# Kernel optimization log

Measured on AMD Instinct MI355X. Metric: run time of the kernel, lower is better.

Reference implementation:

```python
import jax, jax.numpy as jnp
import numpy as np

EPS_RMS = 1e-4   # RunningMeanStd epsilon (mean=0, var=1 at init)
LN_EPS = 1e-5    # torch LayerNorm default
NUM_HEADS = 16


def _layernorm(x, g, b):
    m = x.mean(-1, keepdims=True)
    v = ((x - m) ** 2).mean(-1, keepdims=True)
    return (x - m) / jnp.sqrt(v + LN_EPS) * g + b


def _rms_normalize(a):
    # RunningMeanStd.normalize with mean=0, var=1: clip(a / sqrt(1+eps), -5, 5)
    return jnp.clip(a / jnp.sqrt(1.0 + EPS_RMS), -5.0, 5.0)


def _sinusoidal_pe(pos, d):
    # pos [...,] -> [..., d]; matches torch code: div_term over arange(d//2)
    div = jnp.exp(jnp.arange(d // 2, dtype=jnp.float32) * (-np.log(1000.0) / d))
    ang = pos[..., None] * div                         # [..., d//2]
    pe = jnp.zeros(pos.shape + (d,), dtype=jnp.float32)
    pe = pe.at[..., 0::2].set(jnp.sin(ang))
    pe = pe.at[..., 1::2].set(jnp.cos(ang))
    return pe


def _encoder_layer(xs, mask, Wqkv, bqkv, Wo, bo, g1, be1, g2, be2, Wf1, bf1, Wf2, bf2):
    # post-LN TransformerEncoderLayer with boolean attention mask [B,S,S]
    B, S, D = xs.shape
    hd = D // NUM_HEADS
    qkv = xs @ Wqkv.T + bqkv                           # [B,S,3D]
    q, k, v = jnp.split(qkv, 3, axis=-1)
    q = q.reshape(B, S, NUM_HEADS, hd).transpose(0, 2, 1, 3)
    k = k.reshape(B, S, NUM_HEADS, hd).transpose(0, 2, 1, 3)
    v = v.reshape(B, S, NUM_HEADS, hd).transpose(0, 2, 1, 3)
    scores = jnp.einsum('bhqd,bhkd->bhqk', q, k) / jnp.sqrt(jnp.float32(hd))
    scores = jnp.where(mask[:, None, :, :], -jnp.inf, scores)
    attn = jax.nn.softmax(scores, axis=-1)
    o = jnp.einsum('bhqk,bhkd->bhqd', attn, v).transpose(0, 2, 1, 3).reshape(B, S, D)
    o = o @ Wo.T + bo
    xs = _layernorm(xs + o, g1, be1)
    ff = jax.nn.gelu(xs @ Wf1.T + bf1, approximate=False) @ Wf2.T + bf2
    xs = _layernorm(xs + ff, g2, be2)
    return xs


def reference(x, w, y, W_nail, b_nail, W_cond, b_cond, Wqkv, bqkv, Wo, bo,
              ln1_g, ln1_b, ln2_g, ln2_b, W1, b1, W2, b2, W_ham, b_ham):
    B, Lx = x.shape[0], x.shape[1]
    n_w = w.shape[1] * w.shape[2]
    L = Lx + n_w + 1                                   # total_paragraph_length
    S = L - 1
    D = W_nail.shape[0]

    w_last = w[:, -1]                                  # [B, P, 6]

    # embed_x
    t = jnp.nan_to_num(x[..., 0])
    xc = jnp.nan_to_num(x)
    xx = _rms_normalize(xc)[..., 1:] @ W_nail.T + b_nail   # [B,Lx,D]
    xx = xx + _sinusoidal_pe(t, D)
    x_mask = jnp.isnan(x[..., 0])                      # [B,Lx]

    # embed_w
    wc = jnp.nan_to_num(w)
    wn = _rms_normalize(wc).reshape(B, -1, w.shape[-1])    # [B,Lw*P,6]
    ww = wn @ W_cond.T + b_cond                        # [B,Lw*P,D]

    tgt = jnp.concatenate([xx, ww], axis=1)            # [B,S,D]

    # custom per-batch boolean mask: causal, but columns [0,Lx) follow x padding mask
    causal = jnp.triu(jnp.ones((S, S), dtype=bool), 1)
    mask = jnp.broadcast_to(causal, (B, S, S))
    mask = mask.at[:, :, :Lx].set(x_mask[:, None, :])

    # global positional encoding added only on the w-token segment
    pe_g = _sinusoidal_pe(jnp.arange(L, dtype=jnp.float32), D)  # [L,D]
    tgt = tgt.at[:, Lx:].add(pe_g[Lx:L - 1])

    for i in range(Wqkv.shape[0]):
        tgt = _encoder_layer(tgt, mask, Wqkv[i], bqkv[i], Wo[i], bo[i],
                             ln1_g[i], ln1_b[i], ln2_g[i], ln2_b[i],
                             W1[i], b1[i], W2[i], b2[i])

    y_resid_hat = (tgt[:, -1] @ W_ham.T + b_ham).reshape(B, -1, 6)
    y_resid = jax.lax.stop_gradient(y - w_last)
    loss = jnp.mean((y_resid_hat - y_resid) ** 2)
    return loss


def setup_inputs() -> dict:
    key = jax.random.key(0)
    ks = jax.random.split(key, 16)
    NL, D, FF, HAM = 4, 1024, 4096, 144
    s = 0.02
    return {
        'x': jax.random.normal(ks[0], (8, 512, 64), jnp.float32),
        'w': jax.random.normal(ks[1], (8, 16, 24, 6), jnp.float32),
        'y': jax.random.normal(ks[2], (8, 24, 6), jnp.float32),
        'W_nail': jax.random.normal(ks[3], (D, 63), jnp.float32) * s,
        'b_nail': jnp.zeros((D,), jnp.float32),
        'W_cond': jax.random.normal(ks[4], (D, 6), jnp.float32) * s,
        'b_cond': jnp.zeros((D,), jnp.float32),
        'Wqkv': jax.random.normal(ks[5], (NL, 3 * D, D), jnp.float32) * s,
        'bqkv': jnp.zeros((NL, 3 * D), jnp.float32),
        'Wo': jax.random.normal(ks[6], (NL, D, D), jnp.float32) * s,
        'bo': jnp.zeros((NL, D), jnp.float32),
        'ln1_g': jnp.ones((NL, D), jnp.float32),
        'ln1_b': jnp.zeros((NL, D), jnp.float32),
        'ln2_g': jnp.ones((NL, D), jnp.float32),
        'ln2_b': jnp.zeros((NL, D), jnp.float32),
        'W1': jax.random.normal(ks[7], (NL, FF, D), jnp.float32) * s,
        'b1': jnp.zeros((NL, FF), jnp.float32),
        'W2': jax.random.normal(ks[8], (NL, D, FF), jnp.float32) * s,
        'b2': jnp.zeros((NL, D), jnp.float32),
        'W_ham': jax.random.normal(ks[9], (HAM, D), jnp.float32) * s,
        'b_ham': jnp.zeros((HAM,), jnp.float32),
    }
```

## Files before the change

kernel.cpp:

```cpp
#include <hip/hip_runtime.h>
#include <math.h>


#define B_      8
#define LX_     512
#define NW_     384
#define S_      896
#define D_      1024
#define H_      16
#define HD_     64
#define FF_     4096
#define HAM_    144

#define RMS_SCALE 0.9999500037496876f
#define PE_C     (-6.907755278982137f / 1024.0f)

typedef __bf16 bf16x4 __attribute__((ext_vector_type(4)));
typedef __bf16 bf16x8 __attribute__((ext_vector_type(8)));
typedef float  f32x4  __attribute__((ext_vector_type(4)));

static __device__ __forceinline__ float nan0(float v) { return (v != v) ? 0.0f : v; }

static __device__ __forceinline__ void async_copy16(const __bf16* g, __bf16* l) {
    __builtin_amdgcn_global_load_lds(
        (const __attribute__((address_space(1))) void*)g,
        (__attribute__((address_space(3))) void*)l, 16, 0, 0);
}

static __device__ __forceinline__ float fast_gelu(float x) {
    float x3 = x * x * x;
    float z = 0.7978845608028654f * x + 0.035677408136300125f * x3;
    float az = fabsf(z);
    float e = __expf(2.0f * az);
    float t = 1.0f - 2.0f / (e + 1.0f);
    t = (z < 0.0f) ? -t : t;
    return 0.5f * x * (1.0f + t);
}

__global__ __launch_bounds__(256) void convert4_kernel(
        const float* __restrict__ s0, const float* __restrict__ s1,
        const float* __restrict__ s2, const float* __restrict__ s3,
        __bf16* __restrict__ d0, __bf16* __restrict__ d1,
        __bf16* __restrict__ d2, __bf16* __restrict__ d3) {
    int blk = blockIdx.x;
    const float* src; __bf16* dst; int base;
    if (blk < 3072)      { src = s0; dst = d0; base = blk; }
    else if (blk < 4096) { src = s1; dst = d1; base = blk - 3072; }
    else if (blk < 8192) { src = s2; dst = d2; base = blk - 4096; }
    else                 { src = s3; dst = d3; base = blk - 8192; }
    int i = (base * 256 + threadIdx.x) * 4;
    float4 v = *(const float4*)&src[i];
    bf16x4 o = {(__bf16)v.x, (__bf16)v.y, (__bf16)v.z, (__bf16)v.w};
    *(bf16x4*)&dst[i] = o;
}

__global__ __launch_bounds__(256) void transpose_nail_kernel(
        const float* __restrict__ W_nail, float* __restrict__ WT) {
    int i = blockIdx.x * 256 + threadIdx.x;
    int d = i & 1023, kk = i >> 10;
    WT[kk * 1024 + d] = W_nail[d * 63 + kk];
}

__global__ __launch_bounds__(256) void embed_x_kernel(
        const float* __restrict__ x, const float* __restrict__ WT,
        const float* __restrict__ b_nail, __bf16* __restrict__ tgt_bf,
        int* __restrict__ xmask) {
    int row0 = blockIdx.x * 8;
    int tid = threadIdx.x;
    __shared__ float xn[8][64];
    __shared__ float ts[8];
#pragma unroll
    for (int it = 0; it < 2; ++it) {
        int i = tid + it * 256;
        int r = i >> 6, c = i & 63;
        float vv = x[(size_t)(row0 + r) * 64 + c];
        float v0 = nan0(vv);
        xn[r][c] = fminf(fmaxf(v0 * RMS_SCALE, -5.0f), 5.0f);
        if (c == 0) { ts[r] = v0; xmask[row0 + r] = (vv != vv) ? 1 : 0; }
    }
    __syncthreads();
    int d0 = tid * 4;
    float4 bz = *(const float4*)&b_nail[d0];
    float acc[8][4];
#pragma unroll
    for (int r = 0; r < 8; ++r) {
        acc[r][0] = bz.x; acc[r][1] = bz.y; acc[r][2] = bz.z; acc[r][3] = bz.w;
    }
    for (int k = 0; k < 63; ++k) {
        float4 wv = *(const float4*)&WT[k * 1024 + d0];
#pragma unroll
        for (int r = 0; r < 8; ++r) {
            float xv = xn[r][k + 1];
            acc[r][0] += xv * wv.x; acc[r][1] += xv * wv.y;
            acc[r][2] += xv * wv.z; acc[r][3] += xv * wv.w;
        }
    }
    float div[4];
#pragma unroll
    for (int j = 0; j < 4; ++j)
        div[j] = __expf((float)((d0 + j) >> 1) * PE_C);
#pragma unroll
    for (int r = 0; r < 8; ++r) {
        int row = row0 + r;
        int b = row >> 9, i = row & 511;
        float t = ts[r];
        bf16x4 ob;
#pragma unroll
        for (int j = 0; j < 4; ++j) {
            float ang = t * div[j];
            float pe = ((d0 + j) & 1) ? __cosf(ang) : __sinf(ang);
            ob[j] = (__bf16)(acc[r][j] + pe);
        }
        *(bf16x4*)&tgt_bf[((size_t)b * S_ + i) * D_ + d0] = ob;
    }
}

__global__ __launch_bounds__(256) void embed_w_kernel(
        const float* __restrict__ w, const float* __restrict__ W_cond,
        const float* __restrict__ b_cond, __bf16* __restrict__ tgt_bf) {
    int row = blockIdx.x;
    int b = row / NW_, j = row % NW_;
    const float* wr = w + (long)row * 6;
    float wn[6];
#pragma unroll
    for (int k = 0; k < 6; ++k)
        wn[k] = fminf(fmaxf(nan0(wr[k]) * RMS_SCALE, -5.0f), 5.0f);
    int tid = threadIdx.x;
    int d0 = tid * 4;
    float pos = (float)(LX_ + j);
    bf16x4 ob;
#pragma unroll
    for (int jj = 0; jj < 4; ++jj) {
        int d = d0 + jj;
        float acc = b_cond[d];
        const float* wc = W_cond + (long)d * 6;
#pragma unroll
        for (int k = 0; k < 6; ++k) acc += wn[k] * wc[k];
        float dv = expf((float)(d >> 1) * PE_C);
        float ang = pos * dv;
        ob[jj] = (__bf16)(acc + ((d & 1) ? cosf(ang) : sinf(ang)));
    }
    *(bf16x4*)&tgt_bf[((long)b * S_ + LX_ + j) * D_ + d0] = ob;
}


#define LDA(BUF, MH) do {                                                      \
    _Pragma("unroll")                                                          \
    for (int i_ = 0; i_ < 4; ++i_) {                                           \
        const int row_ = (MH) * 128 + wr * 64 + i_ * 16 + frow;                \
        _Pragma("unroll")                                                      \
        for (int k_ = 0; k_ < 2; ++k_)                                         \
            a[i_][k_] = *(const bf16x8*)&As[BUF][row_ * 64 +                   \
                (((quad + k_ * 4) ^ sf) * 8)];                                 \
    }                                                                          \
} while (0)

#define LDB(BUF, NH) do {                                                      \
    _Pragma("unroll")                                                          \
    for (int j_ = 0; j_ < NJ; ++j_) {                                          \
        const int row_ = (BN == 256)                                           \
            ? ((NH) * 128 + j_ * 16 + wc * 32 + frow)                          \
            : ((NH) * 64 + wc * 16 + frow);                                    \
        _Pragma("unroll")                                                      \
        for (int k_ = 0; k_ < 2; ++k_)                                         \
            b[(NH) * NJ + j_][k_] = *(const bf16x8*)&Bs[BUF][row_ * 64 +       \
                (((quad + k_ * 4) ^ sf) * 8)];                                 \
    }                                                                          \
} while (0)

#define MMA(MH, NH) do {                                                       \
    _Pragma("unroll")                                                          \
    for (int i_ = 0; i_ < 4; ++i_)                                             \
        _Pragma("unroll")                                                      \
        for (int j_ = 0; j_ < NJ; ++j_)                                        \
            _Pragma("unroll")                                                  \
            for (int k_ = 0; k_ < 2; ++k_)                                     \
                acc[(MH) * 4 + i_][(NH) * NJ + j_] =                           \
                    __builtin_amdgcn_mfma_f32_16x16x32_bf16(                   \
                        b[(NH) * NJ + j_][k_], a[i_][k_],                      \
                        acc[(MH) * 4 + i_][(NH) * NJ + j_], 0, 0, 0);          \
} while (0)

#define STAGE_A(BUF, H, KT) do {                                               \
    const __bf16* g_ = Ag + (size_t)((H) * 128) * K + ((size_t)(KT) << 6);     \
    async_copy16(g_, &As[BUF][((H) * 128) * 64 + dst8]);                       \
    async_copy16(g_ + ((size_t)K << 6), &As[BUF][((H) * 128 + 64) * 64 + dst8]); \
} while (0)

#define STAGE_B(BUF, H, KT) do {                                               \
    if constexpr (BN == 256) {                                                 \
        const __bf16* g_ = Wg + (size_t)((H) * 128) * K + ((size_t)(KT) << 6); \
        async_copy16(g_, &Bs[BUF][((H) * 128) * 64 + dst8]);                   \
        async_copy16(g_ + ((size_t)K << 6),                                    \
                     &Bs[BUF][((H) * 128 + 64) * 64 + dst8]);                  \
    } else {                                                                   \
        const __bf16* g_ = Wg + (size_t)((H) * 64) * K + ((size_t)(KT) << 6);  \
        async_copy16(g_, &Bs[BUF][((H) * 64) * 64 + dst8]);                    \
    }                                                                          \
} while (0)

#define PHASE_SYNC() do {                                                      \
    __builtin_amdgcn_sched_barrier(0);                                         \
    __builtin_amdgcn_s_barrier();                                              \
    asm volatile("s_waitcnt lgkmcnt(0)" ::: "memory");                         \
    __builtin_amdgcn_sched_barrier(0);                                         \
} while (0)

#define PHASE_END() do {                                                       \
    __builtin_amdgcn_sched_barrier(0);                                         \
    __builtin_amdgcn_s_barrier();                                              \
} while (0)

#define VM_MAIN do {                                                           \
    if constexpr (BN == 256) { asm volatile("s_waitcnt vmcnt(6)" ::: "memory"); } \
    else                     { asm volatile("s_waitcnt vmcnt(4)" ::: "memory"); } \
} while (0)
#define VM_ZERO asm volatile("s_waitcnt vmcnt(0)" ::: "memory")
#define VM_NONE ((void)0)

#define GTILE(S1, S2, VMOP) do {                                               \
    const int bf_ = t & 1;                                                     \
    LDA(bf_, 0); LDB(bf_, 0);                                                  \
    if (S1) STAGE_A(bf_ ^ 1, 1, t + 1);                                        \
    PHASE_SYNC();                                                              \
    __builtin_amdgcn_s_setprio(1); MMA(0, 0); __builtin_amdgcn_s_setprio(0);   \
    PHASE_END();                                                               \
    LDB(bf_, 1);                                                               \
    if (S2) STAGE_B(bf_, 0, t + 2);                                            \
    PHASE_SYNC();                                                              \
    __builtin_amdgcn_s_setprio(1); MMA(0, 1); __builtin_amdgcn_s_setprio(0);   \
    PHASE_END();                                                               \
    LDA(bf_, 1);                                                               \
    if (S2) STAGE_A(bf_, 0, t + 2);                                            \
    PHASE_SYNC();                                                              \
    __builtin_amdgcn_s_setprio(1); MMA(1, 0); __builtin_amdgcn_s_setprio(0);   \
    PHASE_END();                                                               \
    if (S2) STAGE_B(bf_, 1, t + 2);                                            \
    VMOP;                                                                      \
    PHASE_SYNC();                                                              \
    __builtin_amdgcn_s_setprio(1); MMA(1, 1); __builtin_amdgcn_s_setprio(0);   \
    PHASE_END();                                                               \
} while (0)

template <int BN, int MODE>
__global__ __launch_bounds__(512, 2) void gemm8p(
        const __bf16* __restrict__ A, const __bf16* __restrict__ W,
        const float* __restrict__ bias,
        __bf16* __restrict__ Cb,
        __bf16* __restrict__ Cq, __bf16* __restrict__ Ck, __bf16* __restrict__ Cv,
        int M, int N, int K) {
    constexpr int NI = BN / 64;
    constexpr int NJ = NI / 2;
    static_assert(BN == 256 || BN == 128, "BN");
    __shared__ __attribute__((aligned(16))) __bf16 As[2][256 * 64];
    __shared__ __attribute__((aligned(16))) __bf16 Bs[2][BN * 64];

    const int tid = threadIdx.x;
    const int wave = tid >> 6, lane = tid & 63;
    const int wr = wave >> 2, wc = wave & 3;
    const int frow = lane & 15, quad = lane >> 4;
    const int sf = frow & 7;
    const int m0 = blockIdx.y * 256, n0 = blockIdx.x * BN;

    const int sr = tid >> 3;
    const int scol = ((tid & 7) ^ (sr & 7)) * 8;
    const __bf16* Ag = A + (size_t)(m0 + sr) * K + scol;
    const __bf16* Wg = W + (size_t)(n0 + sr) * K + scol;
    const int dst8 = tid * 8;

    f32x4 acc[8][NI];
#pragma unroll
    for (int i = 0; i < 8; ++i)
#pragma unroll
        for (int j = 0; j < NI; ++j) acc[i][j] = 0.0f;
    bf16x8 a[4][2];
    bf16x8 b[NI][2];

    const int NT = K >> 6;

    STAGE_B(0, 0, 0); STAGE_A(0, 0, 0); STAGE_B(0, 1, 0); STAGE_A(0, 1, 0);
    STAGE_B(1, 0, 1); STAGE_A(1, 0, 1); STAGE_B(1, 1, 1);
    VM_MAIN;
    __builtin_amdgcn_s_barrier();

    int t = 0;
    for (; t < NT - 2; ++t) { GTILE(1, 1, VM_MAIN); }
    GTILE(1, 0, VM_ZERO);
    ++t;
    GTILE(0, 0, VM_NONE);

#pragma unroll
    for (int ni = 0; ni < NI; ++ni) {
        int cg0;
        if constexpr (BN == 256)
            cg0 = n0 + (ni >> 1) * 128 + (ni & 1) * 16 + wc * 32 + quad * 4;
        else
            cg0 = n0 + ni * 64 + wc * 16 + quad * 4;
        float4 bv = *(const float4*)&bias[cg0];
        float bz[4] = {bv.x, bv.y, bv.z, bv.w};
#pragma unroll
        for (int mi = 0; mi < 8; ++mi) {
            int rg = m0 + (mi >> 2) * 128 + wr * 64 + (mi & 3) * 16 + frow;
            float vv[4];
#pragma unroll
            for (int r = 0; r < 4; ++r) {
                float v = acc[mi][ni][r] + bz[r];
                if (MODE == 1) v = fast_gelu(v);
                vv[r] = v;
            }
            if (MODE == 2) {
                int which = cg0 >> 10;
                int h = (cg0 & 1023) >> 6;
                int e = cg0 & 63;
                int bb = rg / S_, s = rg % S_;
                if (which == 2) {
                    size_t vb = ((size_t)bb * H_ + h) * HD_ + e;
#pragma unroll
                    for (int r = 0; r < 4; ++r)
                        Cv[(vb + r) * S_ + s] = (__bf16)vv[r];
                } else {
                    bf16x4 o = {(__bf16)vv[0], (__bf16)vv[1], (__bf16)vv[2], (__bf16)vv[3]};
                    __bf16* dstp = (which == 0) ? Cq : Ck;
                    *(bf16x4*)&dstp[(((size_t)bb * H_ + h) * S_ + s) * HD_ + e] = o;
                }
            } else {
                bf16x4 o = {(__bf16)vv[0], (__bf16)vv[1], (__bf16)vv[2], (__bf16)vv[3]};
                *(bf16x4*)&Cb[(size_t)rg * N + cg0] = o;
            }
        }
    }
}

__global__ __launch_bounds__(512, 2) void gemm2p(
        const __bf16* __restrict__ A, const __bf16* __restrict__ W,
        const float* __restrict__ bias, __bf16* __restrict__ Cb,
        int M, int N, int K) {
    constexpr int BN = 128;
    constexpr int NI = 2, NJ = 1;
    __shared__ __attribute__((aligned(16))) __bf16 As[2][256 * 64];
    __shared__ __attribute__((aligned(16))) __bf16 Bs[2][128 * 64];

    const int tid = threadIdx.x;
    const int wave = tid >> 6, lane = tid & 63;
    const int wr = wave >> 2, wc = wave & 3;
    const int frow = lane & 15, quad = lane >> 4;
    const int sf = frow & 7;

    const int nwg = gridDim.x * gridDim.y;
    int orig = blockIdx.y * gridDim.x + blockIdx.x;
    int tile = orig;
    if ((nwg & 7) == 0) tile = (orig & 7) * (nwg >> 3) + (orig >> 3);
    const int m0 = (tile / gridDim.x) * 256;
    const int n0 = (tile % gridDim.x) * BN;

    const int sr = tid >> 3;
    const int scol = ((tid & 7) ^ (sr & 7)) * 8;
    const __bf16* Ag = A + (size_t)(m0 + sr) * K + scol;
    const __bf16* Wg = W + (size_t)(n0 + sr) * K + scol;
    const int dst8 = tid * 8;

    f32x4 acc[8][NI];
#pragma unroll
    for (int i = 0; i < 8; ++i)
#pragma unroll
        for (int j = 0; j < NI; ++j) acc[i][j] = 0.0f;
    bf16x8 a[4][2];
    bf16x8 b[NI][2];

    const int NT = K >> 6;

#define VM4 asm volatile("s_waitcnt vmcnt(4)" ::: "memory")
#define GTILE2(S1, S2, VMOP) do {                                              \
    const int bf_ = t & 1;                                                     \
            \
    LDA(bf_, 0); LDB(bf_, 0); LDB(bf_, 1);                                     \
    if (S1) STAGE_A(bf_ ^ 1, 1, t + 1);                                        \
    PHASE_SYNC();                                                              \
    __builtin_amdgcn_s_setprio(1); MMA(0, 0); MMA(0, 1);                       \
    __builtin_amdgcn_s_setprio(0);                                             \
    PHASE_END();                                                               \
      \
    LDA(bf_, 1);                                                               \
    if (S2) { STAGE_B(bf_, 0, t + 2); STAGE_B(bf_, 1, t + 2);                  \
              STAGE_A(bf_, 0, t + 2); }                                        \
    VMOP;                                                                      \
    PHASE_SYNC();                                                              \
    __builtin_amdgcn_s_setprio(1); MMA(1, 0); MMA(1, 1);                       \
    __builtin_amdgcn_s_setprio(0);                                             \
    PHASE_END();                                                               \
} while (0)

    STAGE_B(0, 0, 0); STAGE_B(0, 1, 0); STAGE_A(0, 0, 0); STAGE_A(0, 1, 0);
    STAGE_B(1, 0, 1); STAGE_B(1, 1, 1); STAGE_A(1, 0, 1);
    VM4;
    __builtin_amdgcn_s_barrier();

    int t = 0;
    for (; t < NT - 2; ++t) { GTILE2(1, 1, VM4); }
    GTILE2(1, 0, VM_ZERO);
    ++t;
    GTILE2(0, 0, VM_NONE);
#undef GTILE2
#undef VM4

#pragma unroll
    for (int ni = 0; ni < NI; ++ni) {
        int cg0 = n0 + ni * 64 + wc * 16 + quad * 4;
        float4 bv = *(const float4*)&bias[cg0];
        float bz[4] = {bv.x, bv.y, bv.z, bv.w};
#pragma unroll
        for (int mi = 0; mi < 8; ++mi) {
            int rg = m0 + (mi >> 2) * 128 + wr * 64 + (mi & 3) * 16 + frow;
            bf16x4 o;
#pragma unroll
            for (int r = 0; r < 4; ++r) o[r] = (__bf16)(acc[mi][ni][r] + bz[r]);
            *(bf16x4*)&Cb[(size_t)rg * N + cg0] = o;
        }
    }
}

__global__ __launch_bounds__(256) void attn_mfma(
        const __bf16* __restrict__ q, const __bf16* __restrict__ k,
        const __bf16* __restrict__ vt, const int* __restrict__ xmask,
        __bf16* __restrict__ ctx) {
    __shared__ __attribute__((aligned(16))) __bf16 Ks[2][64 * 64];
    __shared__ __attribute__((aligned(16))) __bf16 Vs[2][64 * 64];
    __shared__ __attribute__((aligned(16))) __bf16 Ps[4][16 * 64];
    __shared__ float mb[LX_];
    int tid = threadIdx.x;
    int wave = tid >> 6, lane = tid & 63;
    int frow = lane & 15, quad = lane >> 4;
    int f7 = frow & 7, f3 = frow >> 3;
    int sl0 = (quad ^ f7) * 8;
    int sl1 = ((quad + 4) ^ f7) * 8;

    int blk = blockIdx.x;
    int xcd = blk & 7, slot = blk >> 3;
    int bh = xcd * 16 + slot / 14;
    int qt = slot % 14;
    int b = bh >> 4, h = bh & 15;
    int q0 = qt * 64;
    int q0w = q0 + wave * 16;
    size_t base = (size_t)bh * S_ * HD_;
    size_t vbase = (size_t)bh * HD_ * S_;

    for (int i = tid; i < LX_; i += 256)
        mb[i] = xmask[(b << 9) + i] ? -INFINITY : 0.0f;

    const __bf16* qrow = q + base + (size_t)(q0w + frow) * HD_ + quad * 8;
    bf16x8 aq0 = *(const bf16x8*)qrow;
    bf16x8 aq1 = *(const bf16x8*)(qrow + 32);

    f32x4 o[4];
#pragma unroll
    for (int dt = 0; dt < 4; ++dt) o[dt] = 0.0f;
    float mrow[4] = {-INFINITY, -INFINITY, -INFINITY, -INFINITY};
    float lrow[4] = {0.0f, 0.0f, 0.0f, 0.0f};

    int kend = (q0 >= LX_) ? (q0 + 64) : LX_;
    int NT = kend >> 6;

    int srow = tid >> 3;
    int kcol = ((tid & 7) ^ (srow & 7)) * 8;
    const __bf16* kg = k + base + (size_t)srow * HD_ + kcol;
    const __bf16* vg = vt + vbase + (size_t)srow * S_ + kcol;

#define ASTAGE(BUF, K0) do {                                                   \
    const __bf16* kg_ = kg + (size_t)(K0) * HD_;                               \
    async_copy16(kg_,                  &Ks[BUF][tid * 8]);                     \
    async_copy16(kg_ + 32 * HD_,       &Ks[BUF][2048 + tid * 8]);              \
    const __bf16* vg_ = vg + (K0);                                             \
    async_copy16(vg_,                  &Vs[BUF][tid * 8]);                     \
    async_copy16(vg_ + 32 * S_,        &Vs[BUF][2048 + tid * 8]);              \
} while (0)

    ASTAGE(0, 0);
    __syncthreads();

    for (int t = 0; t < NT; ++t) {
        int buf = t & 1;
        int k0 = t << 6;
        if (t + 1 < NT) {
            ASTAGE(buf ^ 1, k0 + 64);
            asm volatile("s_waitcnt vmcnt(4)" ::: "memory");
        } else {
            asm volatile("s_waitcnt vmcnt(0)" ::: "memory");
        }
        __builtin_amdgcn_s_barrier();
        __builtin_amdgcn_sched_barrier(0);

        f32x4 scr[4];
        __builtin_amdgcn_s_setprio(1);
#pragma unroll
        for (int nt = 0; nt < 4; ++nt) {
            int row = (nt * 16 + frow) * 64;
            bf16x8 bk0 = *(const bf16x8*)&Ks[buf][row + sl0];
            bf16x8 bk1 = *(const bf16x8*)&Ks[buf][row + sl1];
            f32x4 z = 0.0f;
            z = __builtin_amdgcn_mfma_f32_16x16x32_bf16(aq0, bk0, z, 0, 0, 0);
            z = __builtin_amdgcn_mfma_f32_16x16x32_bf16(aq1, bk1, z, 0, 0, 0);
            scr[nt] = z;
        }
        __builtin_amdgcn_s_setprio(0);

        float tmax[4] = {-INFINITY, -INFINITY, -INFINITY, -INFINITY};
#pragma unroll
        for (int nt = 0; nt < 4; ++nt) {
            int kj = k0 + nt * 16 + frow;
            float bias = (kj < LX_) ? mb[kj] : 0.0f;
#pragma unroll
            for (int r = 0; r < 4; ++r) {
                float s = scr[nt][r] * 0.125f + bias;
                if (kj >= LX_ && kj > q0w + quad * 4 + r) s = -INFINITY;
                scr[nt][r] = s;
                tmax[r] = fmaxf(tmax[r], s);
            }
        }
#pragma unroll
        for (int off = 1; off < 16; off <<= 1)
#pragma unroll
            for (int r = 0; r < 4; ++r)
                tmax[r] = fmaxf(tmax[r], __shfl_xor(tmax[r], off, 64));

        float alpha[4], rsum[4];
#pragma unroll
        for (int r = 0; r < 4; ++r) {
            float nm = fmaxf(mrow[r], tmax[r]);
            alpha[r] = (nm == -INFINITY) ? 1.0f : __expf(mrow[r] - nm);
            mrow[r] = nm;
            rsum[r] = 0.0f;
        }
#pragma unroll
        for (int nt = 0; nt < 4; ++nt) {
#pragma unroll
            for (int r = 0; r < 4; ++r) {
                float s = scr[nt][r];
                float p = (s == -INFINITY) ? 0.0f : __expf(s - mrow[r]);
                rsum[r] += p;
                int ql = quad * 4 + r;
                int pslot = ((nt * 2 + f3) ^ (ql & 7)) * 8 + f7;
                Ps[wave][ql * 64 + pslot] = (__bf16)p;
            }
        }
#pragma unroll
        for (int off = 1; off < 16; off <<= 1)
#pragma unroll
            for (int r = 0; r < 4; ++r)
                rsum[r] += __shfl_xor(rsum[r], off, 64);
#pragma unroll
        for (int r = 0; r < 4; ++r)
            lrow[r] = lrow[r] * alpha[r] + rsum[r];
#pragma unroll
        for (int dt = 0; dt < 4; ++dt)
#pragma unroll
            for (int r = 0; r < 4; ++r)
                o[dt][r] *= alpha[r];

        bf16x8 ap0 = *(const bf16x8*)&Ps[wave][frow * 64 + sl0];
        bf16x8 ap1 = *(const bf16x8*)&Ps[wave][frow * 64 + sl1];
        __builtin_amdgcn_s_setprio(1);
#pragma unroll
        for (int dt = 0; dt < 4; ++dt) {
            int row = (dt * 16 + frow) * 64;
            bf16x8 bv0 = *(const bf16x8*)&Vs[buf][row + sl0];
            bf16x8 bv1 = *(const bf16x8*)&Vs[buf][row + sl1];
            o[dt] = __builtin_amdgcn_mfma_f32_16x16x32_bf16(ap0, bv0, o[dt], 0, 0, 0);
            o[dt] = __builtin_amdgcn_mfma_f32_16x16x32_bf16(ap1, bv1, o[dt], 0, 0, 0);
        }
        __builtin_amdgcn_s_setprio(0);
        __builtin_amdgcn_sched_barrier(0);
        __builtin_amdgcn_s_barrier();
    }
#undef ASTAGE

#pragma unroll
    for (int r = 0; r < 4; ++r) {
        float inv = (lrow[r] > 0.0f) ? 1.0f / lrow[r] : 0.0f;
        int qg = q0w + quad * 4 + r;
        size_t ob = ((size_t)b * S_ + qg) * D_ + h * HD_;
#pragma unroll
        for (int dt = 0; dt < 4; ++dt)
            ctx[ob + dt * 16 + frow] = (__bf16)(o[dt][r] * inv);
    }
}

__global__ __launch_bounds__(256) void add_ln_kernel(
        __bf16* __restrict__ xs_bf, const __bf16* __restrict__ o,
        const float* __restrict__ g, const float* __restrict__ bb) {
    long row = blockIdx.x;
    __bf16* xr = xs_bf + row * D_;
    const __bf16* orr = o + row * D_;
    int tid = threadIdx.x;
    bf16x4 a4 = *(const bf16x4*)&xr[tid * 4];
    bf16x4 b4v = *(const bf16x4*)&orr[tid * 4];
    float vv[4];
#pragma unroll
    for (int j = 0; j < 4; ++j) vv[j] = (float)a4[j] + (float)b4v[j];
    float s = vv[0] + vv[1] + vv[2] + vv[3];
    __shared__ float red[4];
    __shared__ float stat;
#pragma unroll
    for (int off = 32; off; off >>= 1) s += __shfl_down(s, off, 64);
    if ((tid & 63) == 0) red[tid >> 6] = s;
    __syncthreads();
    if (tid == 0) stat = (red[0] + red[1] + red[2] + red[3]) * (1.0f / 1024.0f);
    __syncthreads();
    float mean = stat;
    float d[4];
    float s2 = 0.0f;
#pragma unroll
    for (int j = 0; j < 4; ++j) { d[j] = vv[j] - mean; s2 += d[j] * d[j]; }
    __syncthreads();
#pragma unroll
    for (int off = 32; off; off >>= 1) s2 += __shfl_down(s2, off, 64);
    if ((tid & 63) == 0) red[tid >> 6] = s2;
    __syncthreads();
    if (tid == 0) stat = (red[0] + red[1] + red[2] + red[3]) * (1.0f / 1024.0f);
    __syncthreads();
    float inv = 1.0f / sqrtf(stat + 1e-5f);
    float4 gg = *(const float4*)&g[tid * 4];
    float4 bv = *(const float4*)&bb[tid * 4];
    float g4[4] = {gg.x, gg.y, gg.z, gg.w};
    float b4[4] = {bv.x, bv.y, bv.z, bv.w};
    bf16x4 ob;
#pragma unroll
    for (int j = 0; j < 4; ++j) ob[j] = (__bf16)(d[j] * inv * g4[j] + b4[j]);
    *(bf16x4*)&xr[tid * 4] = ob;
}

__global__ __launch_bounds__(256) void head_kernel(
        const __bf16* __restrict__ tgt_bf, const float* __restrict__ W_ham,
        const float* __restrict__ b_ham, float* __restrict__ out) {
    int b = blockIdx.x;
    int tid = threadIdx.x;
    __shared__ float xr[D_];
    const __bf16* row = tgt_bf + ((long)b * S_ + (S_ - 1)) * D_;
    for (int i = tid; i < D_; i += 256) xr[i] = (float)row[i];
    __syncthreads();
    for (int n = tid; n < HAM_; n += 256) {
        float acc = b_ham[n];
        const float* wr = W_ham + (long)n * D_;
        for (int kk = 0; kk < D_; ++kk) acc += xr[kk] * wr[kk];
        out[b * HAM_ + n] = acc;
    }
}

__global__ __launch_bounds__(256) void loss_kernel(
        const float* __restrict__ head_out, const float* __restrict__ y,
        const float* __restrict__ w, float* __restrict__ out) {
    int tid = threadIdx.x;
    float acc = 0.0f;
    for (int i = tid; i < B_ * HAM_; i += 256) {
        int b = i / HAM_, r = i % HAM_;
        float w_last = w[((long)b * 16 + 15) * HAM_ + r];
        float resid = y[i] - w_last;
        float dd = head_out[i] - resid;
        acc += dd * dd;
    }
    __shared__ float red[4];
#pragma unroll
    for (int off = 32; off; off >>= 1) acc += __shfl_down(acc, off, 64);
    if ((tid & 63) == 0) red[tid >> 6] = acc;
    __syncthreads();
    if (tid == 0)
        out[0] = (red[0] + red[1] + red[2] + red[3]) * (1.0f / (B_ * HAM_));
}

extern "C" void kernel_launch(void* const* d_in, const int* in_sizes, int n_in,
                              void* d_out, int out_size, void* d_ws, size_t ws_size,
                              hipStream_t stream) {
    const float* x      = (const float*)d_in[0];
    const float* w      = (const float*)d_in[1];
    const float* y      = (const float*)d_in[2];
    const float* W_nail = (const float*)d_in[3];
    const float* b_nail = (const float*)d_in[4];
    const float* W_cond = (const float*)d_in[5];
    const float* b_cond = (const float*)d_in[6];
    const float* Wqkv   = (const float*)d_in[7];
    const float* bqkv   = (const float*)d_in[8];
    const float* Wo     = (const float*)d_in[9];
    const float* bo     = (const float*)d_in[10];
    const float* ln1_g  = (const float*)d_in[11];
    const float* ln1_b  = (const float*)d_in[12];
    const float* ln2_g  = (const float*)d_in[13];
    const float* ln2_b  = (const float*)d_in[14];
    const float* W1     = (const float*)d_in[15];
    const float* b1     = (const float*)d_in[16];
    const float* W2     = (const float*)d_in[17];
    const float* b2     = (const float*)d_in[18];
    const float* W_ham  = (const float*)d_in[19];
    const float* b_ham  = (const float*)d_in[20];

    float* ws = (float*)d_ws;
    const long SEG = (long)B_ * S_ * D_;
    float*  W_nailT = ws;
    __bf16* tmp_bf = (__bf16*)(ws + SEG);
    __bf16* tgt_bf = (__bf16*)(ws + 2 * SEG);
    __bf16* ctx_bf = (__bf16*)(ws + 2 * SEG + SEG / 2);
    __bf16* qb     = (__bf16*)(ws + 3 * SEG);
    __bf16* kb     = (__bf16*)(ws + 3 * SEG + SEG / 2);
    __bf16* vb     = (__bf16*)(ws + 4 * SEG);
    __bf16* ffh_bf = (__bf16*)(ws + 2 * SEG + SEG / 2);
    __bf16* wbf    = (__bf16*)(ws + 4 * SEG + SEG / 2);
    int*    xmask    = (int*)(ws + 4 * SEG + SEG / 2 + 6291456);
    float*  head_out = ws + 4 * SEG + SEG / 2 + 6291456 + 4096;

    __bf16* wqkv_bf = wbf;
    __bf16* wo_bf   = wbf + 3145728;
    __bf16* w1_bf   = wbf + 4194304;
    __bf16* w2_bf   = wbf + 8388608;

    const int M = B_ * S_;

    transpose_nail_kernel<<<252, 256, 0, stream>>>(W_nail, W_nailT);
    embed_x_kernel<<<B_ * LX_ / 8, 256, 0, stream>>>(x, W_nailT, b_nail, tgt_bf, xmask);
    embed_w_kernel<<<B_ * NW_, 256, 0, stream>>>(w, W_cond, b_cond, tgt_bf);

    for (int L = 0; L < 4; ++L) {
        const int NQ = 3 * D_ * D_, NO = D_ * D_, N1 = FF_ * D_, N2 = D_ * FF_;
        convert4_kernel<<<12288, 256, 0, stream>>>(
            Wqkv + (size_t)L * NQ, Wo + (size_t)L * NO,
            W1 + (size_t)L * N1, W2 + (size_t)L * N2,
            wqkv_bf, wo_bf, w1_bf, w2_bf);

        gemm8p<256, 2><<<dim3(3 * D_ / 256, M / 256), 512, 0, stream>>>(
            tgt_bf, wqkv_bf, bqkv + (size_t)L * 3 * D_,
            nullptr, qb, kb, vb, M, 3 * D_, D_);
        attn_mfma<<<B_ * H_ * (S_ / 64), 256, 0, stream>>>(qb, kb, vb, xmask, ctx_bf);
        gemm2p<<<dim3(D_ / 128, M / 256), 512, 0, stream>>>(
            ctx_bf, wo_bf, bo + (size_t)L * D_, tmp_bf, M, D_, D_);
        add_ln_kernel<<<M, 256, 0, stream>>>(tgt_bf, tmp_bf,
            ln1_g + (size_t)L * D_, ln1_b + (size_t)L * D_);
        gemm8p<256, 1><<<dim3(FF_ / 256, M / 256), 512, 0, stream>>>(
            tgt_bf, w1_bf, b1 + (size_t)L * FF_,
            ffh_bf, nullptr, nullptr, nullptr, M, FF_, D_);
        gemm2p<<<dim3(D_ / 128, M / 256), 512, 0, stream>>>(
            ffh_bf, w2_bf, b2 + (size_t)L * D_, tmp_bf, M, D_, FF_);
        add_ln_kernel<<<M, 256, 0, stream>>>(tgt_bf, tmp_bf,
            ln2_g + (size_t)L * D_, ln2_b + (size_t)L * D_);
    }

    head_kernel<<<B_, 256, 0, stream>>>(tgt_bf, W_ham, b_ham, head_out);
    loss_kernel<<<1, 256, 0, stream>>>(head_out, y, w, (float*)d_out);
}
```

Before: 1.663 ms.

## Load attention K/V straight from global into registers, drop LDS staging

The attention kernel no longer stages K and V tiles through double-buffered shared memory with async copies and block barriers. Each wave now loads its K and V fragments directly from global memory into registers every tile. The mask/causal handling is split into three specialised paths (masked prefix, unmasked, diagonal), and launch bounds now request 3 blocks per CU. This removes LDS traffic and per-tile barriers, but each of the four waves re-reads the same K/V from global/L2 with no prefetch overlap.

```diff
diff --git a/kernel.cpp b/kernel.cpp
--- a/kernel.cpp
+++ b/kernel.cpp
@@ -372,14 +372,12 @@
 #define VM4 asm volatile("s_waitcnt vmcnt(4)" ::: "memory")
 #define GTILE2(S1, S2, VMOP) do {                                              \
     const int bf_ = t & 1;                                                     \
-            \
     LDA(bf_, 0); LDB(bf_, 0); LDB(bf_, 1);                                     \
     if (S1) STAGE_A(bf_ ^ 1, 1, t + 1);                                        \
     PHASE_SYNC();                                                              \
     __builtin_amdgcn_s_setprio(1); MMA(0, 0); MMA(0, 1);                       \
     __builtin_amdgcn_s_setprio(0);                                             \
     PHASE_END();                                                               \
-      \
     LDA(bf_, 1);                                                               \
     if (S2) { STAGE_B(bf_, 0, t + 2); STAGE_B(bf_, 1, t + 2);                  \
               STAGE_A(bf_, 0, t + 2); }                                        \
@@ -419,12 +417,10 @@
     }
 }
 
-__global__ __launch_bounds__(256) void attn_mfma(
+__global__ __launch_bounds__(256, 3) void attn_mfma(
         const __bf16* __restrict__ q, const __bf16* __restrict__ k,
         const __bf16* __restrict__ vt, const int* __restrict__ xmask,
         __bf16* __restrict__ ctx) {
-    __shared__ __attribute__((aligned(16))) __bf16 Ks[2][64 * 64];
-    __shared__ __attribute__((aligned(16))) __bf16 Vs[2][64 * 64];
     __shared__ __attribute__((aligned(16))) __bf16 Ps[4][16 * 64];
     __shared__ float mb[LX_];
     int tid = threadIdx.x;
@@ -446,6 +442,7 @@
 
     for (int i = tid; i < LX_; i += 256)
         mb[i] = xmask[(b << 9) + i] ? -INFINITY : 0.0f;
+    __syncthreads();
 
     const __bf16* qrow = q + base + (size_t)(q0w + frow) * HD_ + quad * 8;
     bf16x8 aq0 = *(const bf16x8*)qrow;
@@ -460,60 +457,63 @@
     int kend = (q0 >= LX_) ? (q0 + 64) : LX_;
     int NT = kend >> 6;
 
-    int srow = tid >> 3;
-    int kcol = ((tid & 7) ^ (srow & 7)) * 8;
-    const __bf16* kg = k + base + (size_t)srow * HD_ + kcol;
-    const __bf16* vg = vt + vbase + (size_t)srow * S_ + kcol;
-
-#define ASTAGE(BUF, K0) do {                                                   \
-    const __bf16* kg_ = kg + (size_t)(K0) * HD_;                               \
-    async_copy16(kg_,                  &Ks[BUF][tid * 8]);                     \
-    async_copy16(kg_ + 32 * HD_,       &Ks[BUF][2048 + tid * 8]);              \
-    const __bf16* vg_ = vg + (K0);                                             \
-    async_copy16(vg_,                  &Vs[BUF][tid * 8]);                     \
-    async_copy16(vg_ + 32 * S_,        &Vs[BUF][2048 + tid * 8]);              \
-} while (0)
-
-    ASTAGE(0, 0);
-    __syncthreads();
+    const __bf16* kg = k + base;
+    const __bf16* vg = vt + vbase;
 
     for (int t = 0; t < NT; ++t) {
-        int buf = t & 1;
         int k0 = t << 6;
-        if (t + 1 < NT) {
-            ASTAGE(buf ^ 1, k0 + 64);
-            asm volatile("s_waitcnt vmcnt(4)" ::: "memory");
-        } else {
-            asm volatile("s_waitcnt vmcnt(0)" ::: "memory");
-        }
-        __builtin_amdgcn_s_barrier();
-        __builtin_amdgcn_sched_barrier(0);
+
+        bf16x8 bk[4][2];
+#pragma unroll
+        for (int nt = 0; nt < 4; ++nt) {
+            const __bf16* kr = kg + (size_t)(k0 + nt * 16 + frow) * HD_ + quad * 8;
+            bk[nt][0] = *(const bf16x8*)kr;
+            bk[nt][1] = *(const bf16x8*)(kr + 32);
+        }
 
         f32x4 scr[4];
         __builtin_amdgcn_s_setprio(1);
 #pragma unroll
         for (int nt = 0; nt < 4; ++nt) {
-            int row = (nt * 16 + frow) * 64;
-            bf16x8 bk0 = *(const bf16x8*)&Ks[buf][row + sl0];
-            bf16x8 bk1 = *(const bf16x8*)&Ks[buf][row + sl1];
             f32x4 z = 0.0f;
-            z = __builtin_amdgcn_mfma_f32_16x16x32_bf16(aq0, bk0, z, 0, 0, 0);
-            z = __builtin_amdgcn_mfma_f32_16x16x32_bf16(aq1, bk1, z, 0, 0, 0);
+            z = __builtin_amdgcn_mfma_f32_16x16x32_bf16(aq0, bk[nt][0], z, 0, 0, 0);
+            z = __builtin_amdgcn_mfma_f32_16x16x32_bf16(aq1, bk[nt][1], z, 0, 0, 0);
             scr[nt] = z;
         }
         __builtin_amdgcn_s_setprio(0);
 
         float tmax[4] = {-INFINITY, -INFINITY, -INFINITY, -INFINITY};
-#pragma unroll
-        for (int nt = 0; nt < 4; ++nt) {
-            int kj = k0 + nt * 16 + frow;
-            float bias = (kj < LX_) ? mb[kj] : 0.0f;
-#pragma unroll
-            for (int r = 0; r < 4; ++r) {
-                float s = scr[nt][r] * 0.125f + bias;
-                if (kj >= LX_ && kj > q0w + quad * 4 + r) s = -INFINITY;
-                scr[nt][r] = s;
-                tmax[r] = fmaxf(tmax[r], s);
+        if (k0 + 64 <= LX_) {
+#pragma unroll
+            for (int nt = 0; nt < 4; ++nt) {
+                float bias = mb[k0 + nt * 16 + frow];
+#pragma unroll
+                for (int r = 0; r < 4; ++r) {
+                    float s = scr[nt][r] * 0.125f + bias;
+                    scr[nt][r] = s;
+                    tmax[r] = fmaxf(tmax[r], s);
+                }
+            }
+        } else if (k0 != q0) {
+#pragma unroll
+            for (int nt = 0; nt < 4; ++nt)
+#pragma unroll
+                for (int r = 0; r < 4; ++r) {
+                    float s = scr[nt][r] * 0.125f;
+                    scr[nt][r] = s;
+                    tmax[r] = fmaxf(tmax[r], s);
+                }
+        } else {
+#pragma unroll
+            for (int nt = 0; nt < 4; ++nt) {
+                int kj = k0 + nt * 16 + frow;
+#pragma unroll
+                for (int r = 0; r < 4; ++r) {
+                    float s = scr[nt][r] * 0.125f;
+                    if (kj > q0w + quad * 4 + r) s = -INFINITY;
+                    scr[nt][r] = s;
+                    tmax[r] = fmaxf(tmax[r], s);
+                }
             }
         }
 #pragma unroll
@@ -542,6 +542,15 @@
                 Ps[wave][ql * 64 + pslot] = (__bf16)p;
             }
         }
+
+        bf16x8 bv[4][2];
+#pragma unroll
+        for (int dt = 0; dt < 4; ++dt) {
+            const __bf16* vr = vg + (size_t)(dt * 16 + frow) * S_ + k0 + quad * 8;
+            bv[dt][0] = *(const bf16x8*)vr;
+            bv[dt][1] = *(const bf16x8*)(vr + 32);
+        }
+
 #pragma unroll
         for (int off = 1; off < 16; off <<= 1)
 #pragma unroll
@@ -561,17 +570,11 @@
         __builtin_amdgcn_s_setprio(1);
 #pragma unroll
         for (int dt = 0; dt < 4; ++dt) {
-            int row = (dt * 16 + frow) * 64;
-            bf16x8 bv0 = *(const bf16x8*)&Vs[buf][row + sl0];
-            bf16x8 bv1 = *(const bf16x8*)&Vs[buf][row + sl1];
-            o[dt] = __builtin_amdgcn_mfma_f32_16x16x32_bf16(ap0, bv0, o[dt], 0, 0, 0);
-            o[dt] = __builtin_amdgcn_mfma_f32_16x16x32_bf16(ap1, bv1, o[dt], 0, 0, 0);
+            o[dt] = __builtin_amdgcn_mfma_f32_16x16x32_bf16(ap0, bv[dt][0], o[dt], 0, 0, 0);
+            o[dt] = __builtin_amdgcn_mfma_f32_16x16x32_bf16(ap1, bv[dt][1], o[dt], 0, 0, 0);
         }
         __builtin_amdgcn_s_setprio(0);
-        __builtin_amdgcn_sched_barrier(0);
-        __builtin_amdgcn_s_barrier();
-    }
-#undef ASTAGE
+    }
 
 #pragma unroll
     for (int r = 0; r < 4; ++r) {
```

Result: slower. 1.921 ms (+15.5%).

## Preload both A halves per GEMM k-tile and specialize attention masking paths

Applied to the files above, without the earlier changes.

The GEMM main loop now reads both A halves from LDS into separate register sets at the start of each k-tile. All four next-stage copies are issued after the first MMA phase, which drops one barrier phase per tile and changes the vmcnt wait depth. Separately, the attention score masking is split into three paths (fully-unmasked prefix, off-diagonal, diagonal) to avoid per-element bias and causal checks. This raises register pressure for the extra A fragments and relies on tile alignment assumptions about LX_ and q0 for the causal branches.

```diff
diff --git a/kernel.cpp b/kernel.cpp
--- a/kernel.cpp
+++ b/kernel.cpp
@@ -155,6 +155,17 @@
     }                                                                          \
 } while (0)
 
+#define LDA2(BUF, MH) do {                                                     \
+    _Pragma("unroll")                                                          \
+    for (int i_ = 0; i_ < 4; ++i_) {                                           \
+        const int row_ = (MH) * 128 + wr * 64 + i_ * 16 + frow;                \
+        _Pragma("unroll")                                                      \
+        for (int k_ = 0; k_ < 2; ++k_)                                         \
+            a2[i_][k_] = *(const bf16x8*)&As[BUF][row_ * 64 +                  \
+                (((quad + k_ * 4) ^ sf) * 8)];                                 \
+    }                                                                          \
+} while (0)
+
 #define LDB(BUF, NH) do {                                                      \
     _Pragma("unroll")                                                          \
     for (int j_ = 0; j_ < NJ; ++j_) {                                          \
@@ -178,6 +189,19 @@
                 acc[(MH) * 4 + i_][(NH) * NJ + j_] =                           \
                     __builtin_amdgcn_mfma_f32_16x16x32_bf16(                   \
                         b[(NH) * NJ + j_][k_], a[i_][k_],                      \
+                        acc[(MH) * 4 + i_][(NH) * NJ + j_], 0, 0, 0);          \
+} while (0)
+
+#define MMA2(MH, NH) do {                                                      \
+    _Pragma("unroll")                                                          \
+    for (int i_ = 0; i_ < 4; ++i_)                                             \
+        _Pragma("unroll")                                                      \
+        for (int j_ = 0; j_ < NJ; ++j_)                                        \
+            _Pragma("unroll")                                                  \
+            for (int k_ = 0; k_ < 2; ++k_)                                     \
+                acc[(MH) * 4 + i_][(NH) * NJ + j_] =                           \
+                    __builtin_amdgcn_mfma_f32_16x16x32_bf16(                   \
+                        b[(NH) * NJ + j_][k_], a2[i_][k_],                     \
                         acc[(MH) * 4 + i_][(NH) * NJ + j_], 0, 0, 0);          \
 } while (0)
 
@@ -365,43 +389,41 @@
 #pragma unroll
         for (int j = 0; j < NI; ++j) acc[i][j] = 0.0f;
     bf16x8 a[4][2];
+    bf16x8 a2[4][2];
     bf16x8 b[NI][2];
 
     const int NT = K >> 6;
 
-#define VM4 asm volatile("s_waitcnt vmcnt(4)" ::: "memory")
-#define GTILE2(S1, S2, VMOP) do {                                              \
+#define VM6 asm volatile("s_waitcnt vmcnt(6)" ::: "memory")
+#define GTILE2(S2, VMOP) do {                                                  \
     const int bf_ = t & 1;                                                     \
-            \
-    LDA(bf_, 0); LDB(bf_, 0); LDB(bf_, 1);                                     \
-    if (S1) STAGE_A(bf_ ^ 1, 1, t + 1);                                        \
+                           \
+    LDA(bf_, 0); LDA2(bf_, 1); LDB(bf_, 0); LDB(bf_, 1);                       \
     PHASE_SYNC();                                                              \
     __builtin_amdgcn_s_setprio(1); MMA(0, 0); MMA(0, 1);                       \
     __builtin_amdgcn_s_setprio(0);                                             \
     PHASE_END();                                                               \
-      \
-    LDA(bf_, 1);                                                               \
+       \
     if (S2) { STAGE_B(bf_, 0, t + 2); STAGE_B(bf_, 1, t + 2);                  \
-              STAGE_A(bf_, 0, t + 2); }                                        \
-    VMOP;                                                                      \
-    PHASE_SYNC();                                                              \
-    __builtin_amdgcn_s_setprio(1); MMA(1, 0); MMA(1, 1);                       \
+              STAGE_A(bf_, 0, t + 2); STAGE_A(bf_, 1, t + 2); }                \
+    VMOP;      \
+    __builtin_amdgcn_s_setprio(1); MMA2(1, 0); MMA2(1, 1);                     \
     __builtin_amdgcn_s_setprio(0);                                             \
     PHASE_END();                                                               \
 } while (0)
 
     STAGE_B(0, 0, 0); STAGE_B(0, 1, 0); STAGE_A(0, 0, 0); STAGE_A(0, 1, 0);
-    STAGE_B(1, 0, 1); STAGE_B(1, 1, 1); STAGE_A(1, 0, 1);
-    VM4;
+    STAGE_B(1, 0, 1); STAGE_B(1, 1, 1); STAGE_A(1, 0, 1); STAGE_A(1, 1, 1);
+    VM6;
     __builtin_amdgcn_s_barrier();
 
     int t = 0;
-    for (; t < NT - 2; ++t) { GTILE2(1, 1, VM4); }
-    GTILE2(1, 0, VM_ZERO);
+    for (; t < NT - 2; ++t) { GTILE2(1, VM6); }
+    GTILE2(0, VM_ZERO);
     ++t;
-    GTILE2(0, 0, VM_NONE);
+    GTILE2(0, VM_NONE);
 #undef GTILE2
-#undef VM4
+#undef VM6
 
 #pragma unroll
     for (int ni = 0; ni < NI; ++ni) {
@@ -504,16 +526,37 @@
         __builtin_amdgcn_s_setprio(0);
 
         float tmax[4] = {-INFINITY, -INFINITY, -INFINITY, -INFINITY};
-#pragma unroll
-        for (int nt = 0; nt < 4; ++nt) {
-            int kj = k0 + nt * 16 + frow;
-            float bias = (kj < LX_) ? mb[kj] : 0.0f;
-#pragma unroll
-            for (int r = 0; r < 4; ++r) {
-                float s = scr[nt][r] * 0.125f + bias;
-                if (kj >= LX_ && kj > q0w + quad * 4 + r) s = -INFINITY;
-                scr[nt][r] = s;
-                tmax[r] = fmaxf(tmax[r], s);
+        if (k0 + 64 <= LX_) {
+#pragma unroll
+            for (int nt = 0; nt < 4; ++nt) {
+                float bias = mb[k0 + nt * 16 + frow];
+#pragma unroll
+                for (int r = 0; r < 4; ++r) {
+                    float s = scr[nt][r] * 0.125f + bias;
+                    scr[nt][r] = s;
+                    tmax[r] = fmaxf(tmax[r], s);
+                }
+            }
+        } else if (k0 != q0) {
+#pragma unroll
+            for (int nt = 0; nt < 4; ++nt)
+#pragma unroll
+                for (int r = 0; r < 4; ++r) {
+                    float s = scr[nt][r] * 0.125f;
+                    scr[nt][r] = s;
+                    tmax[r] = fmaxf(tmax[r], s);
+                }
+        } else {
+#pragma unroll
+            for (int nt = 0; nt < 4; ++nt) {
+                int kj = k0 + nt * 16 + frow;
+#pragma unroll
+                for (int r = 0; r < 4; ++r) {
+                    float s = scr[nt][r] * 0.125f;
+                    if (kj > q0w + quad * 4 + r) s = -INFINITY;
+                    scr[nt][r] = s;
+                    tmax[r] = fmaxf(tmax[r], s);
+                }
             }
         }
 #pragma unroll
```

After: 1.695 ms. No clear change (+1.9%).

## Enlarge attention query tile, skip fully-masked causal tiles, remap GEMM tiles across XCDs

Applied to the files above, without the earlier changes.

The attention kernel now runs 512 threads (8 waves) per block covering 128 query rows, so each staged K/V tile is reused by twice as many queries. The pipeline is reordered to a single barrier per iteration that waits for the current tile and then prefetches the next. Waves whose causal key tile lies entirely beyond their query rows skip all compute, and the mask and causal handling is split into specialised branches. The bf16 GEMM also remaps block indices so neighbouring tiles are grouped per XCD for better L2 locality. The cost is fewer attention blocks, more LDS per block and a load wait that is no longer overlapped with the previous tile's compute.

```diff
diff --git a/kernel.cpp b/kernel.cpp
--- a/kernel.cpp
+++ b/kernel.cpp
@@ -260,7 +260,13 @@
     const int wr = wave >> 2, wc = wave & 3;
     const int frow = lane & 15, quad = lane >> 4;
     const int sf = frow & 7;
-    const int m0 = blockIdx.y * 256, n0 = blockIdx.x * BN;
+
+    const int nwg = gridDim.x * gridDim.y;
+    int orig = blockIdx.y * gridDim.x + blockIdx.x;
+    int tile = orig;
+    if ((nwg & 7) == 0) tile = (orig & 7) * (nwg >> 3) + (orig >> 3);
+    const int m0 = (tile / gridDim.x) * 256;
+    const int n0 = (tile % gridDim.x) * BN;
 
     const int sr = tid >> 3;
     const int scol = ((tid & 7) ^ (sr & 7)) * 8;
@@ -419,13 +425,13 @@
     }
 }
 
-__global__ __launch_bounds__(256) void attn_mfma(
+__global__ __launch_bounds__(512, 4) void attn_mfma(
         const __bf16* __restrict__ q, const __bf16* __restrict__ k,
         const __bf16* __restrict__ vt, const int* __restrict__ xmask,
         __bf16* __restrict__ ctx) {
     __shared__ __attribute__((aligned(16))) __bf16 Ks[2][64 * 64];
     __shared__ __attribute__((aligned(16))) __bf16 Vs[2][64 * 64];
-    __shared__ __attribute__((aligned(16))) __bf16 Ps[4][16 * 64];
+    __shared__ __attribute__((aligned(16))) __bf16 Ps[8][16 * 64];
     __shared__ float mb[LX_];
     int tid = threadIdx.x;
     int wave = tid >> 6, lane = tid & 63;
@@ -436,15 +442,15 @@
 
     int blk = blockIdx.x;
     int xcd = blk & 7, slot = blk >> 3;
-    int bh = xcd * 16 + slot / 14;
-    int qt = slot % 14;
+    int bh = xcd * 16 + slot / 7;
+    int qt = slot % 7;
     int b = bh >> 4, h = bh & 15;
-    int q0 = qt * 64;
+    int q0 = qt * 128;
     int q0w = q0 + wave * 16;
     size_t base = (size_t)bh * S_ * HD_;
     size_t vbase = (size_t)bh * HD_ * S_;
 
-    for (int i = tid; i < LX_; i += 256)
+    for (int i = tid; i < LX_; i += 512)
         mb[i] = xmask[(b << 9) + i] ? -INFINITY : 0.0f;
 
     const __bf16* qrow = q + base + (size_t)(q0w + frow) * HD_ + quad * 8;
@@ -457,21 +463,17 @@
     float mrow[4] = {-INFINITY, -INFINITY, -INFINITY, -INFINITY};
     float lrow[4] = {0.0f, 0.0f, 0.0f, 0.0f};
 
-    int kend = (q0 >= LX_) ? (q0 + 64) : LX_;
+    int kend = (q0 >= LX_) ? (q0 + 128) : LX_;
     int NT = kend >> 6;
 
-    int srow = tid >> 3;
-    int kcol = ((tid & 7) ^ (srow & 7)) * 8;
-    const __bf16* kg = k + base + (size_t)srow * HD_ + kcol;
-    const __bf16* vg = vt + vbase + (size_t)srow * S_ + kcol;
+    int sr = tid >> 3;
+    int kcol = ((tid & 7) ^ (sr & 7)) * 8;
+    const __bf16* kg = k + base + (size_t)sr * HD_ + kcol;
+    const __bf16* vg = vt + vbase + (size_t)sr * S_ + kcol;
 
 #define ASTAGE(BUF, K0) do {                                                   \
-    const __bf16* kg_ = kg + (size_t)(K0) * HD_;                               \
-    async_copy16(kg_,                  &Ks[BUF][tid * 8]);                     \
-    async_copy16(kg_ + 32 * HD_,       &Ks[BUF][2048 + tid * 8]);              \
-    const __bf16* vg_ = vg + (K0);                                             \
-    async_copy16(vg_,                  &Vs[BUF][tid * 8]);                     \
-    async_copy16(vg_ + 32 * S_,        &Vs[BUF][2048 + tid * 8]);              \
+    async_copy16(kg + (size_t)(K0) * HD_, &Ks[BUF][tid * 8]);                  \
+    async_copy16(vg + (K0),               &Vs[BUF][tid * 8]);                  \
 } while (0)
 
     ASTAGE(0, 0);
@@ -480,96 +482,114 @@
     for (int t = 0; t < NT; ++t) {
         int buf = t & 1;
         int k0 = t << 6;
-        if (t + 1 < NT) {
-            ASTAGE(buf ^ 1, k0 + 64);
-            asm volatile("s_waitcnt vmcnt(4)" ::: "memory");
-        } else {
-            asm volatile("s_waitcnt vmcnt(0)" ::: "memory");
-        }
+        asm volatile("s_waitcnt vmcnt(0)" ::: "memory");
         __builtin_amdgcn_s_barrier();
         __builtin_amdgcn_sched_barrier(0);
-
-        f32x4 scr[4];
-        __builtin_amdgcn_s_setprio(1);
-#pragma unroll
-        for (int nt = 0; nt < 4; ++nt) {
-            int row = (nt * 16 + frow) * 64;
-            bf16x8 bk0 = *(const bf16x8*)&Ks[buf][row + sl0];
-            bf16x8 bk1 = *(const bf16x8*)&Ks[buf][row + sl1];
-            f32x4 z = 0.0f;
-            z = __builtin_amdgcn_mfma_f32_16x16x32_bf16(aq0, bk0, z, 0, 0, 0);
-            z = __builtin_amdgcn_mfma_f32_16x16x32_bf16(aq1, bk1, z, 0, 0, 0);
-            scr[nt] = z;
+        if (t + 1 < NT) ASTAGE(buf ^ 1, k0 + 64);
+
+        if (k0 < LX_ || q0w + 15 >= k0) {
+            f32x4 scr[4];
+            __builtin_amdgcn_s_setprio(1);
+#pragma unroll
+            for (int nt = 0; nt < 4; ++nt) {
+                int row = (nt * 16 + frow) * 64;
+                bf16x8 bk0 = *(const bf16x8*)&Ks[buf][row + sl0];
+                bf16x8 bk1 = *(const bf16x8*)&Ks[buf][row + sl1];
+                f32x4 z = 0.0f;
+                z = __builtin_amdgcn_mfma_f32_16x16x32_bf16(aq0, bk0, z, 0, 0, 0);
+                z = __builtin_amdgcn_mfma_f32_16x16x32_bf16(aq1, bk1, z, 0, 0, 0);
+                scr[nt] = z;
+            }
+            __builtin_amdgcn_s_setprio(0);
+
+            float tmax[4] = {-INFINITY, -INFINITY, -INFINITY, -INFINITY};
+            if (k0 < LX_) {
+#pragma unroll
+                for (int nt = 0; nt < 4; ++nt) {
+                    float bias = mb[k0 + nt * 16 + frow];
+#pragma unroll
+                    for (int r = 0; r < 4; ++r) {
+                        float s = scr[nt][r] * 0.125f + bias;
+                        scr[nt][r] = s;
+                        tmax[r] = fmaxf(tmax[r], s);
+                    }
+                }
+            } else if (q0w >= k0 + 64) {
+#pragma unroll
+                for (int nt = 0; nt < 4; ++nt)
+#pragma unroll
+                    for (int r = 0; r < 4; ++r) {
+                        float s = scr[nt][r] * 0.125f;
+                        scr[nt][r] = s;
+                        tmax[r] = fmaxf(tmax[r], s);
+                    }
+            } else {
+#pragma unroll
+                for (int nt = 0; nt < 4; ++nt) {
+                    int kj = k0 + nt * 16 + frow;
+#pragma unroll
+                    for (int r = 0; r < 4; ++r) {
+                        float s = scr[nt][r] * 0.125f;
+                        if (kj > q0w + quad * 4 + r) s = -INFINITY;
+                        scr[nt][r] = s;
+                        tmax[r] = fmaxf(tmax[r], s);
+                    }
+                }
+            }
+#pragma unroll
+            for (int off = 1; off < 16; off <<= 1)
+#pragma unroll
+                for (int r = 0; r < 4; ++r)
+                    tmax[r] = fmaxf(tmax[r], __shfl_xor(tmax[r], off, 64));
+
+            float alpha[4], rsum[4];
+#pragma unroll
+            for (int r = 0; r < 4; ++r) {
+                float nm = fmaxf(mrow[r], tmax[r]);
+                alpha[r] = (nm == -INFINITY) ? 1.0f : __expf(mrow[r] - nm);
+                mrow[r] = nm;
+                rsum[r] = 0.0f;
+            }
+#pragma unroll
+            for (int nt = 0; nt < 4; ++nt) {
+#pragma unroll
+                for (int r = 0; r < 4; ++r) {
+                    float s = scr[nt][r];
+                    float p = (s == -INFINITY) ? 0.0f : __expf(s - mrow[r]);
+                    rsum[r] += p;
+                    int ql = quad * 4 + r;
+                    int pslot = ((nt * 2 + f3) ^ (ql & 7)) * 8 + f7;
+                    Ps[wave][ql * 64 + pslot] = (__bf16)p;
+                }
+            }
+#pragma unroll
+            for (int off = 1; off < 16; off <<= 1)
+#pragma unroll
+                for (int r = 0; r < 4; ++r)
+                    rsum[r] += __shfl_xor(rsum[r], off, 64);
+#pragma unroll
+            for (int r = 0; r < 4; ++r)
+                lrow[r] = lrow[r] * alpha[r] + rsum[r];
+#pragma unroll
+            for (int dt = 0; dt < 4; ++dt)
+#pragma unroll
+                for (int r = 0; r < 4; ++r)
+                    o[dt][r] *= alpha[r];
+
+            bf16x8 ap0 = *(const bf16x8*)&Ps[wave][frow * 64 + sl0];
+            bf16x8 ap1 = *(const bf16x8*)&Ps[wave][frow * 64 + sl1];
+            __builtin_amdgcn_s_setprio(1);
+#pragma unroll
+            for (int dt = 0; dt < 4; ++dt) {
+                int row = (dt * 16 + frow) * 64;
+                bf16x8 bv0 = *(const bf16x8*)&Vs[buf][row + sl0];
+                bf16x8 bv1 = *(const bf16x8*)&Vs[buf][row + sl1];
+                o[dt] = __builtin_amdgcn_mfma_f32_16x16x32_bf16(ap0, bv0, o[dt], 0, 0, 0);
+                o[dt] = __builtin_amdgcn_mfma_f32_16x16x32_bf16(ap1, bv1, o[dt], 0, 0, 0);
+            }
+            __builtin_amdgcn_s_setprio(0);
         }
-        __builtin_amdgcn_s_setprio(0);
-
-        float tmax[4] = {-INFINITY, -INFINITY, -INFINITY, -INFINITY};
-#pragma unroll
-        for (int nt = 0; nt < 4; ++nt) {
-            int kj = k0 + nt * 16 + frow;
-            float bias = (kj < LX_) ? mb[kj] : 0.0f;
-#pragma unroll
-            for (int r = 0; r < 4; ++r) {
-                float s = scr[nt][r] * 0.125f + bias;
-                if (kj >= LX_ && kj > q0w + quad * 4 + r) s = -INFINITY;
-                scr[nt][r] = s;
-                tmax[r] = fmaxf(tmax[r], s);
-            }
-        }
-#pragma unroll
-        for (int off = 1; off < 16; off <<= 1)
-#pragma unroll
-            for (int r = 0; r < 4; ++r)
-                tmax[r] = fmaxf(tmax[r], __shfl_xor(tmax[r], off, 64));
-
-        float alpha[4], rsum[4];
-#pragma unroll
-        for (int r = 0; r < 4; ++r) {
-            float nm = fmaxf(mrow[r], tmax[r]);
-            alpha[r] = (nm == -INFINITY) ? 1.0f : __expf(mrow[r] - nm);
-            mrow[r] = nm;
-            rsum[r] = 0.0f;
-        }
-#pragma unroll
-        for (int nt = 0; nt < 4; ++nt) {
-#pragma unroll
-            for (int r = 0; r < 4; ++r) {
-                float s = scr[nt][r];
-                float p = (s == -INFINITY) ? 0.0f : __expf(s - mrow[r]);
-                rsum[r] += p;
-                int ql = quad * 4 + r;
-                int pslot = ((nt * 2 + f3) ^ (ql & 7)) * 8 + f7;
-                Ps[wave][ql * 64 + pslot] = (__bf16)p;
-            }
-        }
-#pragma unroll
-        for (int off = 1; off < 16; off <<= 1)
-#pragma unroll
-            for (int r = 0; r < 4; ++r)
-                rsum[r] += __shfl_xor(rsum[r], off, 64);
-#pragma unroll
-        for (int r = 0; r < 4; ++r)
-            lrow[r] = lrow[r] * alpha[r] + rsum[r];
-#pragma unroll
-        for (int dt = 0; dt < 4; ++dt)
-#pragma unroll
-            for (int r = 0; r < 4; ++r)
-                o[dt][r] *= alpha[r];
-
-        bf16x8 ap0 = *(const bf16x8*)&Ps[wave][frow * 64 + sl0];
-        bf16x8 ap1 = *(const bf16x8*)&Ps[wave][frow * 64 + sl1];
-        __builtin_amdgcn_s_setprio(1);
-#pragma unroll
-        for (int dt = 0; dt < 4; ++dt) {
-            int row = (dt * 16 + frow) * 64;
-            bf16x8 bv0 = *(const bf16x8*)&Vs[buf][row + sl0];
-            bf16x8 bv1 = *(const bf16x8*)&Vs[buf][row + sl1];
-            o[dt] = __builtin_amdgcn_mfma_f32_16x16x32_bf16(ap0, bv0, o[dt], 0, 0, 0);
-            o[dt] = __builtin_amdgcn_mfma_f32_16x16x32_bf16(ap1, bv1, o[dt], 0, 0, 0);
-        }
-        __builtin_amdgcn_s_setprio(0);
         __builtin_amdgcn_sched_barrier(0);
-        __builtin_amdgcn_s_barrier();
     }
 #undef ASTAGE
 
@@ -726,7 +746,7 @@
         gemm8p<256, 2><<<dim3(3 * D_ / 256, M / 256), 512, 0, stream>>>(
             tgt_bf, wqkv_bf, bqkv + (size_t)L * 3 * D_,
             nullptr, qb, kb, vb, M, 3 * D_, D_);
-        attn_mfma<<<B_ * H_ * (S_ / 64), 256, 0, stream>>>(qb, kb, vb, xmask, ctx_bf);
+        attn_mfma<<<B_ * H_ * (S_ / 128), 512, 0, stream>>>(qb, kb, vb, xmask, ctx_bf);
         gemm2p<<<dim3(D_ / 128, M / 256), 512, 0, stream>>>(
             ctx_bf, wo_bf, bo + (size_t)L * D_, tmp_bf, M, D_, D_);
         add_ln_kernel<<<M, 256, 0, stream>>>(tgt_bf, tmp_bf,
```

Result: no change. 1.638 ms (-1.5%).
